# Kernel tuning notes

Measured on AMD Instinct MI355X. Metric: run time of the kernel, lower is better.

## Reference

```python
import jax, jax.numpy as jnp
import numpy as np

B, H, S, D = 2, 16, 2048, 64  # depth = dmodel / num_heads
DMODEL = H * D


def setup_inputs() -> dict:
    key = jax.random.key(0)
    kq, kk, kv, kw = jax.random.split(key, 4)
    Q = jax.random.normal(kq, (B, H, S, D), dtype=jnp.float32)
    K = jax.random.normal(kk, (B, H, S, D), dtype=jnp.float32)
    V = jax.random.normal(kv, (B, H, S, D), dtype=jnp.float32)
    W = jax.random.normal(kw, (DMODEL, DMODEL), dtype=jnp.float32) * (1.0 / np.sqrt(DMODEL))
    b = jnp.zeros((DMODEL,), dtype=jnp.float32)
    return {"Q": Q, "K": K, "V": V, "W": W, "b": b}


def reference(Q, K, V, W, b):
    depth = Q.shape[-1]
    # scores: (B, H, S, S) -- full score matrix, matching the original math
    scores = jnp.einsum('bhqd,bhkd->bhqk', Q, K) / jnp.sqrt(jnp.float32(depth))
    attn = jax.nn.softmax(scores, axis=-1)
    vals = jnp.einsum('bhqk,bhkd->bhqd', attn, V)          # (B, H, S, D)
    vals = jnp.transpose(vals, (0, 2, 1, 3))               # (B, S, H, D)
    concat = vals.reshape(vals.shape[0], vals.shape[1], -1)  # (B, S, dmodel)
    return concat @ W + b
```

## Files before the change

kernel.cpp:

```cpp
#include <hip/hip_runtime.h>
#include <hip/hip_bf16.h>


typedef float    f32x16  __attribute__((ext_vector_type(16)));
typedef float    f32x4v  __attribute__((ext_vector_type(4)));
typedef __bf16   bf16x8  __attribute__((ext_vector_type(8)));
typedef unsigned short ushort8v __attribute__((ext_vector_type(8)));

#define LOG2E 1.44269504088896f

static constexpr int Bn = 2, Hn = 16, Sn = 2048, Dn = 64, DM = 1024;
static constexpr size_t QKV_ELEMS = (size_t)Bn * Hn * Sn * Dn;

__global__ __launch_bounds__(256) void convert_qkv(
    const float* __restrict__ q, const float* __restrict__ k, const float* __restrict__ v,
    __bf16* __restrict__ qo, __bf16* __restrict__ ko, __bf16* __restrict__ vo) {
  int z = blockIdx.y;
  const float* src = (z == 0) ? q : (z == 1) ? k : v;
  __bf16* dst      = (z == 0) ? qo : (z == 1) ? ko : vo;
  float scale      = (z == 0) ? 0.125f : 1.0f;
  size_t i = ((size_t)blockIdx.x * 256 + threadIdx.x) * 8;
  f32x4v a = *(const f32x4v*)(src + i);
  f32x4v b = *(const f32x4v*)(src + i + 4);
  bf16x8 o;
#pragma unroll
  for (int j = 0; j < 4; ++j) { o[j] = (__bf16)(a[j] * scale); o[4 + j] = (__bf16)(b[j] * scale); }
  *(bf16x8*)(dst + i) = o;
}

__global__ __launch_bounds__(256) void convert_w(const float* __restrict__ w,
                                                 __bf16* __restrict__ wt) {
  __shared__ __bf16 T[64][72];
  const int t = threadIdx.x, r = t >> 2, c0 = (t & 3) * 16;
  const int nt = blockIdx.x * 64, kt = blockIdx.y * 64;
  const float* src = w + (size_t)(kt + r) * DM + nt + c0;
#pragma unroll
  for (int i = 0; i < 4; ++i) {
    f32x4v f = *(const f32x4v*)(src + i * 4);
#pragma unroll
    for (int j = 0; j < 4; ++j) T[r][c0 + i * 4 + j] = (__bf16)f[j];
  }
  __syncthreads();
  bf16x8 o0, o1;
#pragma unroll
  for (int i = 0; i < 8; ++i) { o0[i] = T[c0 + i][r]; o1[i] = T[c0 + 8 + i][r]; }
  __bf16* dst = wt + (size_t)(nt + r) * DM + kt + c0;
  *(bf16x8*)dst = o0;
  *(bf16x8*)(dst + 8) = o1;
}

__global__ __launch_bounds__(256, 2) void attn(
    const __bf16* __restrict__ Qb, const __bf16* __restrict__ Kb,
    const __bf16* __restrict__ Vb, __bf16* __restrict__ Cc) {
  const int tid = threadIdx.x;
  const int wave = tid >> 6, lane = tid & 63;
  const int ln = lane & 31, g = lane >> 5;
  const int qb = blockIdx.x, h = blockIdx.y, bz = blockIdx.z;

  __shared__ __bf16 Ks[64][72];
  __shared__ unsigned short Vt[64][72];
  __shared__ __bf16 Ps[4][32][72];

  const size_t hoff = (size_t)(bz * Hn + h) * Sn * Dn;
  const __bf16* Qp = Qb + hoff + (size_t)(qb * 128 + wave * 32) * Dn;
  const __bf16* Kp = Kb + hoff;
  const unsigned short* Vp = (const unsigned short*)Vb + hoff;

  bf16x8 qf[4];
#pragma unroll
  for (int ks = 0; ks < 4; ++ks)
    qf[ks] = *(const bf16x8*)(Qp + (size_t)ln * Dn + ks * 16 + g * 8);

  f32x16 O0 = {}, O1 = {}, L = {};
  bf16x8 ones;
#pragma unroll
  for (int i = 0; i < 8; ++i) ones[i] = (__bf16)1.0f;

  const int kr = tid >> 2, kc = (tid & 3) * 16;
  const int vu = tid & 7, vv = (tid >> 3) & 7, vw = tid >> 6;
  const int rA = vw * 16 + vv * 2, vc = vu * 8;

  for (int kt = 0; kt < Sn; kt += 64) {
    __syncthreads();
    {
      const __bf16* kp = Kp + (size_t)(kt + kr) * Dn + kc;
      *(bf16x8*)&Ks[kr][kc]     = *(const bf16x8*)kp;
      *(bf16x8*)&Ks[kr][kc + 8] = *(const bf16x8*)(kp + 8);
    }
    {
      const unsigned short* vp = Vp + (size_t)(kt + rA) * Dn + vc;
      ushort8v v0 = *(const ushort8v*)vp;
      ushort8v v1 = *(const ushort8v*)(vp + Dn);
      const int kb = rA >> 3, ko = rA & 7;
#pragma unroll
      for (int j = 0; j < 8; ++j) {
        int d = vc + j;
        int pb = kb ^ ((d >> 3) & 3);
        *(unsigned int*)&Vt[d][pb * 8 + ko] =
            (unsigned int)v0[j] | ((unsigned int)v1[j] << 16);
      }
    }
    __syncthreads();

#pragma unroll
    for (int nt = 0; nt < 2; ++nt) {
      f32x16 s = {};
#pragma unroll
      for (int ks = 0; ks < 4; ++ks) {
        bf16x8 kf = *(const bf16x8*)&Ks[nt * 32 + ln][ks * 16 + g * 8];
        s = __builtin_amdgcn_mfma_f32_32x32x16_bf16(qf[ks], kf, s, 0, 0, 0);
      }
#pragma unroll
      for (int r = 0; r < 16; ++r) {
        float p = __builtin_amdgcn_exp2f(s[r] * LOG2E);
        int row = (r & 3) + ((r >> 2) << 3) + (g << 2);
        Ps[wave][row][nt * 32 + ln] = (__bf16)p;
      }
    }
#pragma unroll
    for (int ks = 0; ks < 4; ++ks) {
      bf16x8 pf = *(const bf16x8*)&Ps[wave][ln][ks * 16 + g * 8];
      L = __builtin_amdgcn_mfma_f32_32x32x16_bf16(pf, ones, L, 0, 0, 0);
      {
        int pb = (2 * ks + g) ^ ((ln >> 3) & 3);
        bf16x8 vf = *(const bf16x8*)&Vt[ln][pb * 8];
        O0 = __builtin_amdgcn_mfma_f32_32x32x16_bf16(pf, vf, O0, 0, 0, 0);
      }
      {
        int pb = (2 * ks + g) ^ (((32 + ln) >> 3) & 3);
        bf16x8 vf = *(const bf16x8*)&Vt[32 + ln][pb * 8];
        O1 = __builtin_amdgcn_mfma_f32_32x32x16_bf16(pf, vf, O1, 0, 0, 0);
      }
    }
  }

  const int q0 = qb * 128 + wave * 32;
#pragma unroll
  for (int r = 0; r < 16; ++r) {
    int row = (r & 3) + ((r >> 2) << 3) + (g << 2);
    float inv = 1.0f / L[r];
    size_t base = (((size_t)bz * Sn + q0 + row) * Hn + h) * Dn;
    Cc[base + ln]      = (__bf16)(O0[r] * inv);
    Cc[base + 32 + ln] = (__bf16)(O1[r] * inv);
  }
}

__global__ __launch_bounds__(256, 2) void proj(
    const __bf16* __restrict__ A, const __bf16* __restrict__ Wt,
    const float* __restrict__ bias, float* __restrict__ out) {
  const int tid = threadIdx.x, wave = tid >> 6, lane = tid & 63;
  const int ln = lane & 31, g = lane >> 5;
  const int bm = blockIdx.x, bn = blockIdx.y;
  __shared__ __bf16 As[128][72];
  __shared__ __bf16 Bs[64][72];
  const int ar = tid >> 1, ac = (tid & 1) * 32;
  const int br = tid >> 2, bc = (tid & 3) * 16;
  f32x16 acc0 = {}, acc1 = {};
  const __bf16* Ap = A + (size_t)(bm * 128) * DM;
  const __bf16* Wp = Wt + (size_t)(bn * 64) * DM;

  for (int kt = 0; kt < DM; kt += 64) {
    __syncthreads();
#pragma unroll
    for (int i = 0; i < 4; ++i)
      *(bf16x8*)&As[ar][ac + i * 8] =
          *(const bf16x8*)(Ap + (size_t)ar * DM + kt + ac + i * 8);
    {
      const __bf16* wp = Wp + (size_t)br * DM + kt + bc;
      *(bf16x8*)&Bs[br][bc]     = *(const bf16x8*)wp;
      *(bf16x8*)&Bs[br][bc + 8] = *(const bf16x8*)(wp + 8);
    }
    __syncthreads();
#pragma unroll
    for (int ks = 0; ks < 4; ++ks) {
      bf16x8 af = *(const bf16x8*)&As[wave * 32 + ln][ks * 16 + g * 8];
      bf16x8 b0 = *(const bf16x8*)&Bs[ln][ks * 16 + g * 8];
      bf16x8 b1 = *(const bf16x8*)&Bs[32 + ln][ks * 16 + g * 8];
      acc0 = __builtin_amdgcn_mfma_f32_32x32x16_bf16(af, b0, acc0, 0, 0, 0);
      acc1 = __builtin_amdgcn_mfma_f32_32x32x16_bf16(af, b1, acc1, 0, 0, 0);
    }
  }
  float bv0 = bias[bn * 64 + ln], bv1 = bias[bn * 64 + 32 + ln];
#pragma unroll
  for (int r = 0; r < 16; ++r) {
    int row = bm * 128 + wave * 32 + (r & 3) + ((r >> 2) << 3) + (g << 2);
    out[(size_t)row * DM + bn * 64 + ln]      = acc0[r] + bv0;
    out[(size_t)row * DM + bn * 64 + 32 + ln] = acc1[r] + bv1;
  }
}

extern "C" void kernel_launch(void* const* d_in, const int* in_sizes, int n_in,
                              void* d_out, int out_size, void* d_ws, size_t ws_size,
                              hipStream_t stream) {
  const float* Q = (const float*)d_in[0];
  const float* K = (const float*)d_in[1];
  const float* V = (const float*)d_in[2];
  const float* W = (const float*)d_in[3];
  const float* b = (const float*)d_in[4];
  float* out = (float*)d_out;

  __bf16* ws = (__bf16*)d_ws;
  __bf16* Qb = ws;
  __bf16* Kb = Qb + QKV_ELEMS;
  __bf16* Vb = Kb + QKV_ELEMS;
  __bf16* Cc = Vb + QKV_ELEMS;
  __bf16* Wt = Cc + QKV_ELEMS;

  convert_qkv<<<dim3((unsigned)(QKV_ELEMS / (256 * 8)), 3, 1), 256, 0, stream>>>(
      Q, K, V, Qb, Kb, Vb);
  convert_w<<<dim3(DM / 64, DM / 64, 1), 256, 0, stream>>>(W, Wt);
  attn<<<dim3(Sn / 128, Hn, Bn), 256, 0, stream>>>(Qb, Kb, Vb, Cc);
  proj<<<dim3(Bn * Sn / 128, DM / 64, 1), 256, 0, stream>>>(Cc, Wt, b, out);
}
```

Before: 185.3 us.

## Pre-transpose V, compute transposed scores in registers, double-buffer attention and projection

V is now transposed into a d-major bf16 layout by a separate conversion kernel, and the log2e factor is folded into the Q scale. Attention computes S^T so probabilities stay in registers: lanes exchange halves through shuffles instead of an LDS round trip, and the row sum is accumulated in scalar form instead of through an extra MFMA against a ones vector. Both attention and projection now double-buffer their LDS tiles, prefetching the next tile into registers while computing the current one. The attention output is staged through LDS so global stores are coalesced 16-byte writes. In exchange LDS use per block doubles, which may reduce occupancy, and an extra conversion kernel is launched.

```diff
diff --git a/kernel.cpp b/kernel.cpp
--- a/kernel.cpp
+++ b/kernel.cpp
@@ -2,23 +2,29 @@
 #include <hip/hip_bf16.h>
 
 
-typedef float    f32x16  __attribute__((ext_vector_type(16)));
-typedef float    f32x4v  __attribute__((ext_vector_type(4)));
-typedef __bf16   bf16x8  __attribute__((ext_vector_type(8)));
-typedef unsigned short ushort8v __attribute__((ext_vector_type(8)));
-
-#define LOG2E 1.44269504088896f
+typedef float  f32x16 __attribute__((ext_vector_type(16)));
+typedef float  f32x4v __attribute__((ext_vector_type(4)));
+typedef __bf16 bf16x8 __attribute__((ext_vector_type(8)));
+typedef __bf16 bf16x4 __attribute__((ext_vector_type(4)));
 
 static constexpr int Bn = 2, Hn = 16, Sn = 2048, Dn = 64, DM = 1024;
 static constexpr size_t QKV_ELEMS = (size_t)Bn * Hn * Sn * Dn;
 
-__global__ __launch_bounds__(256) void convert_qkv(
-    const float* __restrict__ q, const float* __restrict__ k, const float* __restrict__ v,
-    __bf16* __restrict__ qo, __bf16* __restrict__ ko, __bf16* __restrict__ vo) {
-  int z = blockIdx.y;
-  const float* src = (z == 0) ? q : (z == 1) ? k : v;
-  __bf16* dst      = (z == 0) ? qo : (z == 1) ? ko : vo;
-  float scale      = (z == 0) ? 0.125f : 1.0f;
+#define QSCALE 0.18033688011112042f
+
+static __device__ __forceinline__ unsigned pack2(float a, float b) {
+  union { __bf16 h; unsigned short s; } ua, ub;
+  ua.h = (__bf16)a; ub.h = (__bf16)b;
+  return (unsigned)ua.s | ((unsigned)ub.s << 16);
+}
+
+__global__ __launch_bounds__(256) void convert_qk(
+    const float* __restrict__ q, const float* __restrict__ k,
+    __bf16* __restrict__ qo, __bf16* __restrict__ ko) {
+  const int z = blockIdx.y;
+  const float* src = z ? k : q;
+  __bf16* dst      = z ? ko : qo;
+  const float scale = z ? 1.0f : QSCALE;
   size_t i = ((size_t)blockIdx.x * 256 + threadIdx.x) * 8;
   f32x4v a = *(const f32x4v*)(src + i);
   f32x4v b = *(const f32x4v*)(src + i + 4);
@@ -26,6 +32,28 @@
 #pragma unroll
   for (int j = 0; j < 4; ++j) { o[j] = (__bf16)(a[j] * scale); o[4 + j] = (__bf16)(b[j] * scale); }
   *(bf16x8*)(dst + i) = o;
+}
+
+__global__ __launch_bounds__(256) void convert_vt(const float* __restrict__ v,
+                                                  __bf16* __restrict__ vt) {
+  __shared__ __bf16 T[64][72];
+  const int t = threadIdx.x, r = t >> 2, c0 = (t & 3) * 16;
+  const int kv0 = blockIdx.x * 64, bh = blockIdx.y;
+  const float* src = v + ((size_t)bh * Sn + kv0 + r) * Dn + c0;
+#pragma unroll
+  for (int i = 0; i < 4; ++i) {
+    f32x4v f = *(const f32x4v*)(src + i * 4);
+#pragma unroll
+    for (int j = 0; j < 4; ++j) T[r][c0 + i * 4 + j] = (__bf16)f[j];
+  }
+  __syncthreads();
+  const int dr = t >> 2, k0 = (t & 3) * 16;
+  bf16x8 o0, o1;
+#pragma unroll
+  for (int i = 0; i < 8; ++i) { o0[i] = T[k0 + i][dr]; o1[i] = T[k0 + 8 + i][dr]; }
+  __bf16* dst = vt + ((size_t)bh * Dn + dr) * Sn + kv0 + k0;
+  *(bf16x8*)dst = o0;
+  *(bf16x8*)(dst + 8) = o1;
 }
 
 __global__ __launch_bounds__(256) void convert_w(const float* __restrict__ w,
@@ -51,97 +79,118 @@
 
 __global__ __launch_bounds__(256, 2) void attn(
     const __bf16* __restrict__ Qb, const __bf16* __restrict__ Kb,
-    const __bf16* __restrict__ Vb, __bf16* __restrict__ Cc) {
+    const __bf16* __restrict__ Vtg, __bf16* __restrict__ Cc) {
   const int tid = threadIdx.x;
   const int wave = tid >> 6, lane = tid & 63;
   const int ln = lane & 31, g = lane >> 5;
   const int qb = blockIdx.x, h = blockIdx.y, bz = blockIdx.z;
 
-  __shared__ __bf16 Ks[64][72];
-  __shared__ unsigned short Vt[64][72];
-  __shared__ __bf16 Ps[4][32][72];
+  __shared__ __bf16 Ks[2][64][72];
+  __shared__ __bf16 Vs[2][64][72];
 
   const size_t hoff = (size_t)(bz * Hn + h) * Sn * Dn;
   const __bf16* Qp = Qb + hoff + (size_t)(qb * 128 + wave * 32) * Dn;
   const __bf16* Kp = Kb + hoff;
-  const unsigned short* Vp = (const unsigned short*)Vb + hoff;
+  const __bf16* Vp = Vtg + hoff;
 
   bf16x8 qf[4];
 #pragma unroll
   for (int ks = 0; ks < 4; ++ks)
     qf[ks] = *(const bf16x8*)(Qp + (size_t)ln * Dn + ks * 16 + g * 8);
 
-  f32x16 O0 = {}, O1 = {}, L = {};
-  bf16x8 ones;
-#pragma unroll
-  for (int i = 0; i < 8; ++i) ones[i] = (__bf16)1.0f;
-
-  const int kr = tid >> 2, kc = (tid & 3) * 16;
-  const int vu = tid & 7, vv = (tid >> 3) & 7, vw = tid >> 6;
-  const int rA = vw * 16 + vv * 2, vc = vu * 8;
-
-  for (int kt = 0; kt < Sn; kt += 64) {
-    __syncthreads();
-    {
-      const __bf16* kp = Kp + (size_t)(kt + kr) * Dn + kc;
-      *(bf16x8*)&Ks[kr][kc]     = *(const bf16x8*)kp;
-      *(bf16x8*)&Ks[kr][kc + 8] = *(const bf16x8*)(kp + 8);
-    }
-    {
-      const unsigned short* vp = Vp + (size_t)(kt + rA) * Dn + vc;
-      ushort8v v0 = *(const ushort8v*)vp;
-      ushort8v v1 = *(const ushort8v*)(vp + Dn);
-      const int kb = rA >> 3, ko = rA & 7;
-#pragma unroll
-      for (int j = 0; j < 8; ++j) {
-        int d = vc + j;
-        int pb = kb ^ ((d >> 3) & 3);
-        *(unsigned int*)&Vt[d][pb * 8 + ko] =
-            (unsigned int)v0[j] | ((unsigned int)v1[j] << 16);
+  const int sr = tid >> 2, sc = (tid & 3) * 16;
+  bf16x8 k0r, k1r, v0r, v1r;
+  {
+    const __bf16* kp = Kp + (size_t)sr * Dn + sc;
+    k0r = *(const bf16x8*)kp; k1r = *(const bf16x8*)(kp + 8);
+    const __bf16* vp = Vp + (size_t)sr * Sn + sc;
+    v0r = *(const bf16x8*)vp; v1r = *(const bf16x8*)(vp + 8);
+  }
+
+  f32x16 O0 = {}, O1 = {};
+  float Lown = 0.0f;
+
+  for (int kt = 0; kt < Sn / 64; ++kt) {
+    const int buf = kt & 1;
+    *(bf16x8*)&Ks[buf][sr][sc]     = k0r;
+    *(bf16x8*)&Ks[buf][sr][sc + 8] = k1r;
+    *(bf16x8*)&Vs[buf][sr][sc]     = v0r;
+    *(bf16x8*)&Vs[buf][sr][sc + 8] = v1r;
+    __syncthreads();
+
+    if (kt < Sn / 64 - 1) {
+      const __bf16* kp = Kp + (size_t)((kt + 1) * 64 + sr) * Dn + sc;
+      k0r = *(const bf16x8*)kp; k1r = *(const bf16x8*)(kp + 8);
+      const __bf16* vp = Vp + (size_t)sr * Sn + (kt + 1) * 64 + sc;
+      v0r = *(const bf16x8*)vp; v1r = *(const bf16x8*)(vp + 8);
+    }
+
+    float p[32];
+#pragma unroll
+    for (int mt = 0; mt < 2; ++mt) {
+      f32x16 s = {};
+#pragma unroll
+      for (int ks = 0; ks < 4; ++ks) {
+        bf16x8 kf = *(const bf16x8*)&Ks[buf][mt * 32 + ln][ks * 16 + g * 8];
+        s = __builtin_amdgcn_mfma_f32_32x32x16_bf16(kf, qf[ks], s, 0, 0, 0);
       }
-    }
-    __syncthreads();
-
-#pragma unroll
-    for (int nt = 0; nt < 2; ++nt) {
-      f32x16 s = {};
-#pragma unroll
-      for (int ks = 0; ks < 4; ++ks) {
-        bf16x8 kf = *(const bf16x8*)&Ks[nt * 32 + ln][ks * 16 + g * 8];
-        s = __builtin_amdgcn_mfma_f32_32x32x16_bf16(qf[ks], kf, s, 0, 0, 0);
-      }
-#pragma unroll
-      for (int r = 0; r < 16; ++r) {
-        float p = __builtin_amdgcn_exp2f(s[r] * LOG2E);
-        int row = (r & 3) + ((r >> 2) << 3) + (g << 2);
-        Ps[wave][row][nt * 32 + ln] = (__bf16)p;
-      }
-    }
-#pragma unroll
-    for (int ks = 0; ks < 4; ++ks) {
-      bf16x8 pf = *(const bf16x8*)&Ps[wave][ln][ks * 16 + g * 8];
-      L = __builtin_amdgcn_mfma_f32_32x32x16_bf16(pf, ones, L, 0, 0, 0);
-      {
-        int pb = (2 * ks + g) ^ ((ln >> 3) & 3);
-        bf16x8 vf = *(const bf16x8*)&Vt[ln][pb * 8];
-        O0 = __builtin_amdgcn_mfma_f32_32x32x16_bf16(pf, vf, O0, 0, 0, 0);
-      }
-      {
-        int pb = (2 * ks + g) ^ (((32 + ln) >> 3) & 3);
-        bf16x8 vf = *(const bf16x8*)&Vt[32 + ln][pb * 8];
-        O1 = __builtin_amdgcn_mfma_f32_32x32x16_bf16(pf, vf, O1, 0, 0, 0);
-      }
-    }
-  }
-
-  const int q0 = qb * 128 + wave * 32;
-#pragma unroll
-  for (int r = 0; r < 16; ++r) {
-    int row = (r & 3) + ((r >> 2) << 3) + (g << 2);
-    float inv = 1.0f / L[r];
-    size_t base = (((size_t)bz * Sn + q0 + row) * Hn + h) * Dn;
-    Cc[base + ln]      = (__bf16)(O0[r] * inv);
-    Cc[base + 32 + ln] = (__bf16)(O1[r] * inv);
+#pragma unroll
+      for (int r = 0; r < 16; ++r) p[mt * 16 + r] = __builtin_amdgcn_exp2f(s[r]);
+    }
+    float sum = 0.0f;
+#pragma unroll
+    for (int r = 0; r < 32; ++r) sum += p[r];
+    Lown += sum;
+
+    unsigned w[16];
+#pragma unroll
+    for (int t = 0; t < 8; ++t) {
+      w[t]     = pack2(p[2 * t], p[2 * t + 1]);
+      w[8 + t] = pack2(p[16 + 2 * t], p[16 + 2 * t + 1]);
+    }
+
+#pragma unroll
+    for (int s4 = 0; s4 < 4; ++s4) {
+      const int wb = (s4 >> 1) * 8 + (s4 & 1) * 4;
+      unsigned xs0 = g ? w[wb + 0] : w[wb + 2];
+      unsigned xs1 = g ? w[wb + 1] : w[wb + 3];
+      unsigned x0 = (unsigned)__shfl_xor((int)xs0, 32);
+      unsigned x1 = (unsigned)__shfl_xor((int)xs1, 32);
+      union { unsigned u[4]; bf16x8 v; } pu;
+      pu.u[0] = g ? x0 : w[wb + 0];
+      pu.u[1] = g ? x1 : w[wb + 1];
+      pu.u[2] = g ? w[wb + 2] : x0;
+      pu.u[3] = g ? w[wb + 3] : x1;
+      bf16x8 vf0 = *(const bf16x8*)&Vs[buf][ln][s4 * 16 + g * 8];
+      bf16x8 vf1 = *(const bf16x8*)&Vs[buf][32 + ln][s4 * 16 + g * 8];
+      O0 = __builtin_amdgcn_mfma_f32_32x32x16_bf16(vf0, pu.v, O0, 0, 0, 0);
+      O1 = __builtin_amdgcn_mfma_f32_32x32x16_bf16(vf1, pu.v, O1, 0, 0, 0);
+    }
+    __syncthreads();
+  }
+
+  const float Lfull = Lown + __shfl_xor(Lown, 32);
+  const float inv = 1.0f / Lfull;
+  __bf16* Osb = ((__bf16*)Ks) + wave * 32 * 72;
+#pragma unroll
+  for (int mtD = 0; mtD < 2; ++mtD) {
+#pragma unroll
+    for (int a = 0; a < 4; ++a) {
+      const f32x16 O = mtD ? O1 : O0;
+      bf16x4 t4;
+#pragma unroll
+      for (int c = 0; c < 4; ++c) t4[c] = (__bf16)(O[4 * a + c] * inv);
+      *(bf16x4*)(Osb + ln * 72 + mtD * 32 + 8 * a + 4 * g) = t4;
+    }
+  }
+  const int q0w = qb * 128 + wave * 32;
+#pragma unroll
+  for (int i = 0; i < 4; ++i) {
+    const int rq = i * 8 + (lane >> 3);
+    const int c8 = (lane & 7) * 8;
+    bf16x8 o = *(const bf16x8*)(Osb + rq * 72 + c8);
+    size_t base = (((size_t)bz * Sn + q0w + rq) * Hn + h) * Dn + c8;
+    *(bf16x8*)&Cc[base] = o;
   }
 }
 
@@ -151,34 +200,48 @@
   const int tid = threadIdx.x, wave = tid >> 6, lane = tid & 63;
   const int ln = lane & 31, g = lane >> 5;
   const int bm = blockIdx.x, bn = blockIdx.y;
-  __shared__ __bf16 As[128][72];
-  __shared__ __bf16 Bs[64][72];
+  __shared__ __bf16 As[2][128][72];
+  __shared__ __bf16 Bs[2][64][72];
   const int ar = tid >> 1, ac = (tid & 1) * 32;
   const int br = tid >> 2, bc = (tid & 3) * 16;
   f32x16 acc0 = {}, acc1 = {};
   const __bf16* Ap = A + (size_t)(bm * 128) * DM;
   const __bf16* Wp = Wt + (size_t)(bn * 64) * DM;
 
-  for (int kt = 0; kt < DM; kt += 64) {
-    __syncthreads();
-#pragma unroll
-    for (int i = 0; i < 4; ++i)
-      *(bf16x8*)&As[ar][ac + i * 8] =
-          *(const bf16x8*)(Ap + (size_t)ar * DM + kt + ac + i * 8);
-    {
-      const __bf16* wp = Wp + (size_t)br * DM + kt + bc;
-      *(bf16x8*)&Bs[br][bc]     = *(const bf16x8*)wp;
-      *(bf16x8*)&Bs[br][bc + 8] = *(const bf16x8*)(wp + 8);
-    }
-    __syncthreads();
+  bf16x8 a0, a1, a2, a3, b0, b1;
+  {
+    const __bf16* ap = Ap + (size_t)ar * DM + ac;
+    a0 = *(const bf16x8*)ap;        a1 = *(const bf16x8*)(ap + 8);
+    a2 = *(const bf16x8*)(ap + 16); a3 = *(const bf16x8*)(ap + 24);
+    const __bf16* wp = Wp + (size_t)br * DM + bc;
+    b0 = *(const bf16x8*)wp; b1 = *(const bf16x8*)(wp + 8);
+  }
+
+  for (int kt = 0; kt < DM / 64; ++kt) {
+    const int buf = kt & 1;
+    *(bf16x8*)&As[buf][ar][ac]      = a0;
+    *(bf16x8*)&As[buf][ar][ac + 8]  = a1;
+    *(bf16x8*)&As[buf][ar][ac + 16] = a2;
+    *(bf16x8*)&As[buf][ar][ac + 24] = a3;
+    *(bf16x8*)&Bs[buf][br][bc]      = b0;
+    *(bf16x8*)&Bs[buf][br][bc + 8]  = b1;
+    __syncthreads();
+    if (kt < DM / 64 - 1) {
+      const __bf16* ap = Ap + (size_t)ar * DM + (kt + 1) * 64 + ac;
+      a0 = *(const bf16x8*)ap;        a1 = *(const bf16x8*)(ap + 8);
+      a2 = *(const bf16x8*)(ap + 16); a3 = *(const bf16x8*)(ap + 24);
+      const __bf16* wp = Wp + (size_t)br * DM + (kt + 1) * 64 + bc;
+      b0 = *(const bf16x8*)wp; b1 = *(const bf16x8*)(wp + 8);
+    }
 #pragma unroll
     for (int ks = 0; ks < 4; ++ks) {
-      bf16x8 af = *(const bf16x8*)&As[wave * 32 + ln][ks * 16 + g * 8];
-      bf16x8 b0 = *(const bf16x8*)&Bs[ln][ks * 16 + g * 8];
-      bf16x8 b1 = *(const bf16x8*)&Bs[32 + ln][ks * 16 + g * 8];
-      acc0 = __builtin_amdgcn_mfma_f32_32x32x16_bf16(af, b0, acc0, 0, 0, 0);
-      acc1 = __builtin_amdgcn_mfma_f32_32x32x16_bf16(af, b1, acc1, 0, 0, 0);
-    }
+      bf16x8 af  = *(const bf16x8*)&As[buf][wave * 32 + ln][ks * 16 + g * 8];
+      bf16x8 wf0 = *(const bf16x8*)&Bs[buf][ln][ks * 16 + g * 8];
+      bf16x8 wf1 = *(const bf16x8*)&Bs[buf][32 + ln][ks * 16 + g * 8];
+      acc0 = __builtin_amdgcn_mfma_f32_32x32x16_bf16(af, wf0, acc0, 0, 0, 0);
+      acc1 = __builtin_amdgcn_mfma_f32_32x32x16_bf16(af, wf1, acc1, 0, 0, 0);
+    }
+    __syncthreads();
   }
   float bv0 = bias[bn * 64 + ln], bv1 = bias[bn * 64 + 32 + ln];
 #pragma unroll
@@ -199,16 +262,16 @@
   const float* b = (const float*)d_in[4];
   float* out = (float*)d_out;
 
-  __bf16* ws = (__bf16*)d_ws;
-  __bf16* Qb = ws;
-  __bf16* Kb = Qb + QKV_ELEMS;
-  __bf16* Vb = Kb + QKV_ELEMS;
-  __bf16* Cc = Vb + QKV_ELEMS;
-  __bf16* Wt = Cc + QKV_ELEMS;
-
-  convert_qkv<<<dim3((unsigned)(QKV_ELEMS / (256 * 8)), 3, 1), 256, 0, stream>>>(
-      Q, K, V, Qb, Kb, Vb);
+  __bf16* ws  = (__bf16*)d_ws;
+  __bf16* Qb  = ws;
+  __bf16* Kb  = Qb + QKV_ELEMS;
+  __bf16* Vtg = Kb + QKV_ELEMS;
+  __bf16* Cc  = Vtg + QKV_ELEMS;
+  __bf16* Wt  = Cc + QKV_ELEMS;
+
+  convert_qk<<<dim3((unsigned)(QKV_ELEMS / (256 * 8)), 2, 1), 256, 0, stream>>>(Q, K, Qb, Kb);
+  convert_vt<<<dim3(Sn / 64, Bn * Hn, 1), 256, 0, stream>>>(V, Vtg);
   convert_w<<<dim3(DM / 64, DM / 64, 1), 256, 0, stream>>>(W, Wt);
-  attn<<<dim3(Sn / 128, Hn, Bn), 256, 0, stream>>>(Qb, Kb, Vb, Cc);
+  attn<<<dim3(Sn / 128, Hn, Bn), 256, 0, stream>>>(Qb, Kb, Vtg, Cc);
   proj<<<dim3(Bn * Sn / 128, DM / 64, 1), 256, 0, stream>>>(Cc, Wt, b, out);
 }
```

Result: faster. 167.8 us (-9.4%).
